# Performance work log

Measured on AMD Instinct MI355X. Metric: run time of the kernel, lower is better.

Reference implementation:

```python
import jax, jax.numpy as jnp
import numpy as np

SCALE = 2
STRIDE = 1


def setup_inputs() -> dict:
    key = jax.random.key(0)
    kx, kw, kb = jax.random.split(key, 3)
    B, Cin, H, W = 16, 128, 64, 64
    Cout, kh, kw_ = 128, 3, 3
    N = Cout * Cin * kh * kw_
    bound = 1.0 / np.sqrt(N)
    x = jax.random.normal(kx, (B, Cin, H, W), dtype=jnp.float32)
    weight = jax.random.uniform(kw, (Cout, Cin, kh, kw_), dtype=jnp.float32,
                                minval=-bound, maxval=bound)
    bias = jax.random.uniform(kb, (Cout,), dtype=jnp.float32,
                              minval=-bound, maxval=bound)
    return {"x": x, "weight": weight, "bias": bias}


def reference(x, weight, bias):
    # Nearest-neighbor upsample: each input pixel replicated SCALE x SCALE.
    up = jnp.repeat(jnp.repeat(x, SCALE, axis=2), SCALE, axis=3)  # [B,C,H*s,W*s]
    # Conv2d (cross-correlation, no padding), same math as unfold + matmul.
    out = jax.lax.conv_general_dilated(
        up, weight,
        window_strides=(STRIDE, STRIDE),
        padding="VALID",
        dimension_numbers=("NCHW", "OIHW", "NCHW"),
    )
    return out + bias[None, :, None, None]
```

## Files before the change

kernel.cpp:

```cpp
#include <hip/hip_runtime.h>
#include <hip/hip_bf16.h>
#include <stdint.h>


#define B_    16
#define CIN   128
#define HIN   64
#define WIN   64
#define COUT  128
#define HO    126
#define WO    126
#define M_TOT (B_ * 63 * 63)
#define BM    64
#define KTILES 16
#define AS_K  520

typedef __bf16 bf16;
typedef __bf16 bf16x8 __attribute__((ext_vector_type(8)));
typedef float  floatx4 __attribute__((ext_vector_type(4)));

__global__ void prep_weights(const float* __restrict__ w, bf16* __restrict__ wb) {
    int idx = blockIdx.x * 256 + threadIdx.x;
    if (idx >= 4 * KTILES * COUT * 32) return;
    int k32 = idx & 31;
    int o   = (idx >> 5) & 127;
    int par = (idx >> 12) & 3;
    int kt  = idx >> 14;
    int k = kt * 32 + k32;
    int c = k >> 2, u = (k >> 1) & 1, v = k & 1;
    int a = par >> 1, bp = par & 1;
    int dy0, dy1, ndy, dx0, dx1, ndx;
    if (u == 0) { if (a == 0) { dy0 = 0; dy1 = 1; ndy = 2; } else { dy0 = 0; dy1 = 0; ndy = 1; } }
    else        { if (a == 0) { dy0 = 2; dy1 = 2; ndy = 1; } else { dy0 = 1; dy1 = 2; ndy = 2; } }
    if (v == 0) { if (bp == 0) { dx0 = 0; dx1 = 1; ndx = 2; } else { dx0 = 0; dx1 = 0; ndx = 1; } }
    else        { if (bp == 0) { dx0 = 2; dx1 = 2; ndx = 1; } else { dx0 = 1; dx1 = 2; ndx = 2; } }
    const float* wp = w + (o * CIN + c) * 9;
    float s = wp[dy0 * 3 + dx0];
    if (ndx == 2) s += wp[dy0 * 3 + dx1];
    if (ndy == 2) { s += wp[dy1 * 3 + dx0]; if (ndx == 2) s += wp[dy1 * 3 + dx1]; }
    wb[idx] = (bf16)s;
}

__global__ __launch_bounds__(512, 4)
void upconv_gemm(const float* __restrict__ x, const bf16* __restrict__ wb,
                 const float* __restrict__ bias, float* __restrict__ out) {
    __shared__ bf16 As[BM * AS_K];
    float* Ld = reinterpret_cast<float*>(As);

    const int t    = threadIdx.x;
    const int lane = t & 63;
    const int wid  = t >> 6;
    const int a    = wid >> 2;
    const int oq   = wid & 3;
    const int quad = lane >> 4;
    const int l15  = lane & 15;
    const int kq   = quad * 8;

    const int m0 = blockIdx.x * BM;

    {
        const int ml = lane;
        const int m_mine = m0 + ml;
        const bool mvalid = (m_mine < M_TOT);
        int b_ = 0, p_ = 0, q_ = 0;
        if (mvalid) { b_ = m_mine / 3969; int rr = m_mine - b_ * 3969; p_ = rr / 63; q_ = rr - p_ * 63; }
        const float* xbase = x + ((b_ * CIN) * HIN + p_) * WIN + q_;

        #pragma unroll
        for (int j = 0; j < 8; ++j) {
            const int c0 = wid * 16 + 2 * j;
            float f0[4] = {0.f, 0.f, 0.f, 0.f}, f1[4] = {0.f, 0.f, 0.f, 0.f};
            if (mvalid) {
                const float* pa = xbase + c0 * (HIN * WIN);
                f0[0] = pa[0]; f0[1] = pa[1]; f0[2] = pa[WIN]; f0[3] = pa[WIN + 1];
                const float* pb = pa + (HIN * WIN);
                f1[0] = pb[0]; f1[1] = pb[1]; f1[2] = pb[WIN]; f1[3] = pb[WIN + 1];
            }
            bf16x8 v;
            v[0] = (bf16)f0[0]; v[1] = (bf16)f0[1]; v[2] = (bf16)f0[2]; v[3] = (bf16)f0[3];
            v[4] = (bf16)f1[0]; v[5] = (bf16)f1[1]; v[6] = (bf16)f1[2]; v[7] = (bf16)f1[3];
            const int g = wid * 8 + j;
            *(bf16x8*)&As[ml * AS_K + g * 8] = v;
        }
    }
    __syncthreads();

    const bf16* wwave = wb + ((a * 2) * COUT + oq * 32 + l15) * 32 + kq;

    floatx4 acc[2][4][2] = {};

    #pragma unroll
    for (int kt = 0; kt < KTILES; ++kt) {
        bf16x8 af[4], wf[2][2];
        #pragma unroll
        for (int i = 0; i < 4; ++i)
            af[i] = *(const bf16x8*)&As[(i * 16 + l15) * AS_K + kt * 32 + kq];
        #pragma unroll
        for (int bp = 0; bp < 2; ++bp)
            #pragma unroll
            for (int nt = 0; nt < 2; ++nt)
                wf[bp][nt] = *(const bf16x8*)(wwave
                    + (kt * 4 * COUT + bp * COUT + nt * 16) * 32);
        #pragma unroll
        for (int bp = 0; bp < 2; ++bp)
            #pragma unroll
            for (int mt = 0; mt < 4; ++mt)
                #pragma unroll
                for (int nt = 0; nt < 2; ++nt)
                    acc[bp][mt][nt] = __builtin_amdgcn_mfma_f32_16x16x32_bf16(
                        wf[bp][nt], af[mt], acc[bp][mt][nt], 0, 0, 0);
    }

    const int b_base = m0 / 3969;
    const int rr0 = m0 - b_base * 3969;
    const int p0  = rr0 / 63;
    const int q   = lane;

    #pragma unroll
    for (int ap = 0; ap < 2; ++ap) {
        __syncthreads();

        if (a == ap) {
            #pragma unroll
            for (int bp = 0; bp < 2; ++bp)
                #pragma unroll
                for (int mt = 0; mt < 4; ++mt)
                    #pragma unroll
                    for (int nt = 0; nt < 2; ++nt)
                        #pragma unroll
                        for (int ri = 0; ri < 4; ++ri) {
                            const int o   = oq * 32 + nt * 16 + quad * 4 + ri;
                            const int mlx = (mt * 16 + l15) ^ (quad << 4);
                            Ld[(o * 2 + bp) * 64 + mlx] = acc[bp][mt][nt][ri];
                        }
        }
        __syncthreads();

        for (int i = 0; i < 32; ++i) {
            const int rid = wid * 32 + i;
            const int o   = rid >> 1;
            const int pi  = rid & 1;
            int b = b_base, p = p0 + pi;
            if (p > 62) { b += 1; p = 0; }
            if (b >= B_) continue;
            const int base_m = b * 3969 + p * 63;
            const float bo = bias[o];
            const int m_lane = base_m + q;
            const bool val = (q < 63) && (m_lane >= m0) && (m_lane < m0 + BM) && (m_lane < M_TOT);
            if (val) {
                const int mloc = m_lane - m0;
                const int xsw  = ((o >> 2) & 3) << 4;
                const float v0 = Ld[(o * 2 + 0) * 64 + (mloc ^ xsw)];
                const float v1 = Ld[(o * 2 + 1) * 64 + (mloc ^ xsw)];
                const int y = 2 * p + ap;
                float* dst = out + b * (COUT * HO * WO) + o * (HO * WO) + y * WO + 2 * q;
                *(float2*)dst = make_float2(v0 + bo, v1 + bo);
            }
        }
    }
}

extern "C" void kernel_launch(void* const* d_in, const int* in_sizes, int n_in,
                              void* d_out, int out_size, void* d_ws, size_t ws_size,
                              hipStream_t stream) {
    const float* x    = (const float*)d_in[0];
    const float* w    = (const float*)d_in[1];
    const float* bias = (const float*)d_in[2];
    float* out = (float*)d_out;
    bf16* wb = (bf16*)d_ws;

    prep_weights<<<(4 * KTILES * COUT * 32 + 255) / 256, 256, 0, stream>>>(w, wb);

    dim3 grid((M_TOT + BM - 1) / BM);
    upconv_gemm<<<grid, 512, 0, stream>>>(x, wb, bias, out);
}
```

Baseline: 214.3 us.

## Double-buffer weights and activations in LDS with async global-to-LDS loads

Replaces the up-front full-K activation staging and the direct global weight loads with a double-buffered K loop. Each iteration streams the next weight tile into LDS with global_load_lds, using an XOR swizzle, and prefetches the next 8 input channels into registers, writing them into the alternate LDS buffer after the MFMAs. The aim is to overlap global memory latency with the matrix math and to cut per-wave redundant global weight reads. In exchange it adds a __syncthreads per K tile, uses more LDS (about 74KB), which may lower occupancy, and relies on the swizzle matching between prep layout and reads.

Measured after the change: 213.6 us. Within noise of the previous version (-0.3%).

```diff
diff --git a/kernel.cpp b/kernel.cpp
--- a/kernel.cpp
+++ b/kernel.cpp
@@ -13,9 +13,12 @@
 #define M_TOT (B_ * 63 * 63)
 #define BM    64
 #define KTILES 16
-#define AS_K  520
+#define WS_ELEMS 16384
+#define AS_STRIDE 40
+#define AS_ELEMS (64 * AS_STRIDE)
 
 typedef __bf16 bf16;
+typedef __bf16 bf16x4 __attribute__((ext_vector_type(4)));
 typedef __bf16 bf16x8 __attribute__((ext_vector_type(8)));
 typedef float  floatx4 __attribute__((ext_vector_type(4)));
 
@@ -44,8 +47,10 @@
 __global__ __launch_bounds__(512, 4)
 void upconv_gemm(const float* __restrict__ x, const bf16* __restrict__ wb,
                  const float* __restrict__ bias, float* __restrict__ out) {
-    __shared__ bf16 As[BM * AS_K];
-    float* Ld = reinterpret_cast<float*>(As);
+    __shared__ __align__(16) char smem[2 * WS_ELEMS * 2 + 2 * AS_ELEMS * 2];
+    bf16*  Ws  = (bf16*)smem;
+    bf16*  Asl = (bf16*)(smem + 2 * WS_ELEMS * 2);
+    float* Ld  = (float*)smem;
 
     const int t    = threadIdx.x;
     const int lane = t & 63;
@@ -58,49 +63,65 @@
 
     const int m0 = blockIdx.x * BM;
 
+    const int m_mine = m0 + lane;
+    const bool mvalid = (m_mine < M_TOT);
+    int b_ = 0, p_ = 0, q_ = 0;
+    if (mvalid) { b_ = m_mine / 3969; int rr = m_mine - b_ * 3969; p_ = rr / 63; q_ = rr - p_ * 63; }
+    const float* xpl = x + ((b_ * CIN + wid) * HIN + p_) * WIN + q_;
+
+    const int go_base = a * 1024 + oq * 128 + l15 * 4 + quad;
+
     {
-        const int ml = lane;
-        const int m_mine = m0 + ml;
-        const bool mvalid = (m_mine < M_TOT);
-        int b_ = 0, p_ = 0, q_ = 0;
-        if (mvalid) { b_ = m_mine / 3969; int rr = m_mine - b_ * 3969; p_ = rr / 63; q_ = rr - p_ * 63; }
-        const float* xbase = x + ((b_ * CIN) * HIN + p_) * WIN + q_;
-
-        #pragma unroll
-        for (int j = 0; j < 8; ++j) {
-            const int c0 = wid * 16 + 2 * j;
-            float f0[4] = {0.f, 0.f, 0.f, 0.f}, f1[4] = {0.f, 0.f, 0.f, 0.f};
-            if (mvalid) {
-                const float* pa = xbase + c0 * (HIN * WIN);
-                f0[0] = pa[0]; f0[1] = pa[1]; f0[2] = pa[WIN]; f0[3] = pa[WIN + 1];
-                const float* pb = pa + (HIN * WIN);
-                f1[0] = pb[0]; f1[1] = pb[1]; f1[2] = pb[WIN]; f1[3] = pb[WIN + 1];
-            }
-            bf16x8 v;
-            v[0] = (bf16)f0[0]; v[1] = (bf16)f0[1]; v[2] = (bf16)f0[2]; v[3] = (bf16)f0[3];
-            v[4] = (bf16)f1[0]; v[5] = (bf16)f1[1]; v[6] = (bf16)f1[2]; v[7] = (bf16)f1[3];
-            const int g = wid * 8 + j;
-            *(bf16x8*)&As[ml * AS_K + g * 8] = v;
-        }
+        #pragma unroll
+        for (int i = 0; i < 4; ++i) {
+            const int j  = i * 512 + t;
+            const int js = j ^ ((j >> 3) & 7);
+            __builtin_amdgcn_global_load_lds(
+                (const __attribute__((address_space(1))) uint32_t*)(const void*)(wb + js * 8),
+                (__attribute__((address_space(3))) uint32_t*)(void*)(Ws + j * 8),
+                16, 0, 0);
+        }
+        float f0 = 0.f, f1 = 0.f, f2 = 0.f, f3 = 0.f;
+        if (mvalid) { f0 = xpl[0]; f1 = xpl[1]; f2 = xpl[WIN]; f3 = xpl[WIN + 1]; }
+        bf16x4 v; v[0] = (bf16)f0; v[1] = (bf16)f1; v[2] = (bf16)f2; v[3] = (bf16)f3;
+        *(bf16x4*)&Asl[lane * AS_STRIDE + wid * 4] = v;
     }
     __syncthreads();
 
-    const bf16* wwave = wb + ((a * 2) * COUT + oq * 32 + l15) * 32 + kq;
-
     floatx4 acc[2][4][2] = {};
 
-    #pragma unroll
+    #pragma unroll 2
     for (int kt = 0; kt < KTILES; ++kt) {
+        const int cur = kt & 1;
+        const int nxt = cur ^ 1;
+
+        float f0 = 0.f, f1 = 0.f, f2 = 0.f, f3 = 0.f;
+        if (kt < KTILES - 1) {
+            #pragma unroll
+            for (int i = 0; i < 4; ++i) {
+                const int j  = i * 512 + t;
+                const int js = j ^ ((j >> 3) & 7);
+                __builtin_amdgcn_global_load_lds(
+                    (const __attribute__((address_space(1))) uint32_t*)(const void*)(wb + (kt + 1) * WS_ELEMS + js * 8),
+                    (__attribute__((address_space(3))) uint32_t*)(void*)(Ws + nxt * WS_ELEMS + j * 8),
+                    16, 0, 0);
+            }
+            const float* pa = xpl + (kt + 1) * 8 * (HIN * WIN);
+            if (mvalid) { f0 = pa[0]; f1 = pa[1]; f2 = pa[WIN]; f3 = pa[WIN + 1]; }
+        }
+
         bf16x8 af[4], wf[2][2];
         #pragma unroll
         for (int i = 0; i < 4; ++i)
-            af[i] = *(const bf16x8*)&As[(i * 16 + l15) * AS_K + kt * 32 + kq];
+            af[i] = *(const bf16x8*)&Asl[cur * AS_ELEMS + (i * 16 + l15) * AS_STRIDE + kq];
         #pragma unroll
         for (int bp = 0; bp < 2; ++bp)
             #pragma unroll
-            for (int nt = 0; nt < 2; ++nt)
-                wf[bp][nt] = *(const bf16x8*)(wwave
-                    + (kt * 4 * COUT + bp * COUT + nt * 16) * 32);
+            for (int nt = 0; nt < 2; ++nt) {
+                const int go = go_base + bp * 512 + nt * 64;
+                const int s  = go ^ ((go >> 3) & 7);
+                wf[bp][nt] = *(const bf16x8*)&Ws[cur * WS_ELEMS + s * 8];
+            }
         #pragma unroll
         for (int bp = 0; bp < 2; ++bp)
             #pragma unroll
@@ -109,6 +130,12 @@
                 for (int nt = 0; nt < 2; ++nt)
                     acc[bp][mt][nt] = __builtin_amdgcn_mfma_f32_16x16x32_bf16(
                         wf[bp][nt], af[mt], acc[bp][mt][nt], 0, 0, 0);
+
+        if (kt < KTILES - 1) {
+            bf16x4 v; v[0] = (bf16)f0; v[1] = (bf16)f1; v[2] = (bf16)f2; v[3] = (bf16)f3;
+            *(bf16x4*)&Asl[nxt * AS_ELEMS + lane * AS_STRIDE + wid * 4] = v;
+        }
+        __syncthreads();
     }
 
     const int b_base = m0 / 3969;
```

## Align GEMM tiles to output rows and simplify epilogue stores

Applied to the files above, without the earlier changes.

Each block now handles exactly one input row (63 pixels) of one image instead of a flat 64-pixel M tile. This removes the per-lane div/mod index math and the tile-straddling validity checks. The epilogue adds bias in registers and writes float2 pairs to an LDS buffer padded to 65 entries per channel. The copy-out loop is unrolled over 16 channels per wave, with no row-boundary branching, and uses nontemporal stores. One of the 64 M lanes in each tile is wasted, and the block count rises slightly.

Result: no change. 212.4 us (-0.9%).

```diff
diff --git a/kernel.cpp b/kernel.cpp
--- a/kernel.cpp
+++ b/kernel.cpp
@@ -10,14 +10,14 @@
 #define COUT  128
 #define HO    126
 #define WO    126
-#define M_TOT (B_ * 63 * 63)
-#define BM    64
+#define BM    63
 #define KTILES 16
 #define AS_K  520
 
 typedef __bf16 bf16;
 typedef __bf16 bf16x8 __attribute__((ext_vector_type(8)));
 typedef float  floatx4 __attribute__((ext_vector_type(4)));
+typedef float  floatx2 __attribute__((ext_vector_type(2)));
 
 __global__ void prep_weights(const float* __restrict__ w, bf16* __restrict__ wb) {
     int idx = blockIdx.x * 256 + threadIdx.x;
@@ -44,8 +44,8 @@
 __global__ __launch_bounds__(512, 4)
 void upconv_gemm(const float* __restrict__ x, const bf16* __restrict__ wb,
                  const float* __restrict__ bias, float* __restrict__ out) {
-    __shared__ bf16 As[BM * AS_K];
-    float* Ld = reinterpret_cast<float*>(As);
+    __shared__ bf16 As[64 * AS_K];
+    floatx2* Ld2 = reinterpret_cast<floatx2*>(As);
 
     const int t    = threadIdx.x;
     const int lane = t & 63;
@@ -56,15 +56,13 @@
     const int l15  = lane & 15;
     const int kq   = quad * 8;
 
-    const int m0 = blockIdx.x * BM;
+    const int bid = blockIdx.x;
+    const int b   = bid / 63;
+    const int p   = bid - b * 63;
 
     {
-        const int ml = lane;
-        const int m_mine = m0 + ml;
-        const bool mvalid = (m_mine < M_TOT);
-        int b_ = 0, p_ = 0, q_ = 0;
-        if (mvalid) { b_ = m_mine / 3969; int rr = m_mine - b_ * 3969; p_ = rr / 63; q_ = rr - p_ * 63; }
-        const float* xbase = x + ((b_ * CIN) * HIN + p_) * WIN + q_;
+        const bool mvalid = (lane < 63);
+        const float* xbase = x + ((b * CIN) * HIN + p) * WIN + lane;
 
         #pragma unroll
         for (int j = 0; j < 8; ++j) {
@@ -80,7 +78,7 @@
             v[0] = (bf16)f0[0]; v[1] = (bf16)f0[1]; v[2] = (bf16)f0[2]; v[3] = (bf16)f0[3];
             v[4] = (bf16)f1[0]; v[5] = (bf16)f1[1]; v[6] = (bf16)f1[2]; v[7] = (bf16)f1[3];
             const int g = wid * 8 + j;
-            *(bf16x8*)&As[ml * AS_K + g * 8] = v;
+            *(bf16x8*)&As[lane * AS_K + g * 8] = v;
         }
     }
     __syncthreads();
@@ -111,10 +109,14 @@
                         wf[bp][nt], af[mt], acc[bp][mt][nt], 0, 0, 0);
     }
 
-    const int b_base = m0 / 3969;
-    const int rr0 = m0 - b_base * 3969;
-    const int p0  = rr0 / 63;
-    const int q   = lane;
+    float bv[2][4];
+    #pragma unroll
+    for (int nt = 0; nt < 2; ++nt)
+        #pragma unroll
+        for (int ri = 0; ri < 4; ++ri)
+            bv[nt][ri] = bias[oq * 32 + nt * 16 + quad * 4 + ri];
+
+    const int y0 = 2 * p;
 
     #pragma unroll
     for (int ap = 0; ap < 2; ++ap) {
@@ -122,39 +124,28 @@
 
         if (a == ap) {
             #pragma unroll
-            for (int bp = 0; bp < 2; ++bp)
+            for (int mt = 0; mt < 4; ++mt)
                 #pragma unroll
-                for (int mt = 0; mt < 4; ++mt)
+                for (int nt = 0; nt < 2; ++nt)
                     #pragma unroll
-                    for (int nt = 0; nt < 2; ++nt)
-                        #pragma unroll
-                        for (int ri = 0; ri < 4; ++ri) {
-                            const int o   = oq * 32 + nt * 16 + quad * 4 + ri;
-                            const int mlx = (mt * 16 + l15) ^ (quad << 4);
-                            Ld[(o * 2 + bp) * 64 + mlx] = acc[bp][mt][nt][ri];
-                        }
+                    for (int ri = 0; ri < 4; ++ri) {
+                        const int o = oq * 32 + nt * 16 + quad * 4 + ri;
+                        const int q = mt * 16 + l15;
+                        floatx2 r;
+                        r[0] = acc[0][mt][nt][ri] + bv[nt][ri];
+                        r[1] = acc[1][mt][nt][ri] + bv[nt][ri];
+                        Ld2[o * 65 + q] = r;
+                    }
         }
         __syncthreads();
 
-        for (int i = 0; i < 32; ++i) {
-            const int rid = wid * 32 + i;
-            const int o   = rid >> 1;
-            const int pi  = rid & 1;
-            int b = b_base, p = p0 + pi;
-            if (p > 62) { b += 1; p = 0; }
-            if (b >= B_) continue;
-            const int base_m = b * 3969 + p * 63;
-            const float bo = bias[o];
-            const int m_lane = base_m + q;
-            const bool val = (q < 63) && (m_lane >= m0) && (m_lane < m0 + BM) && (m_lane < M_TOT);
-            if (val) {
-                const int mloc = m_lane - m0;
-                const int xsw  = ((o >> 2) & 3) << 4;
-                const float v0 = Ld[(o * 2 + 0) * 64 + (mloc ^ xsw)];
-                const float v1 = Ld[(o * 2 + 1) * 64 + (mloc ^ xsw)];
-                const int y = 2 * p + ap;
-                float* dst = out + b * (COUT * HO * WO) + o * (HO * WO) + y * WO + 2 * q;
-                *(float2*)dst = make_float2(v0 + bo, v1 + bo);
+        #pragma unroll
+        for (int i = 0; i < 16; ++i) {
+            const int o = wid * 16 + i;
+            if (lane < 63) {
+                floatx2 v = Ld2[o * 65 + lane];
+                float* dst = out + ((b * COUT + o) * HO + (y0 + ap)) * WO + 2 * lane;
+                __builtin_nontemporal_store(v, (floatx2*)dst);
             }
         }
     }
@@ -171,6 +162,5 @@
 
     prep_weights<<<(4 * KTILES * COUT * 32 + 255) / 256, 256, 0, stream>>>(w, wb);
 
-    dim3 grid((M_TOT + BM - 1) / BM);
-    upconv_gemm<<<grid, 512, 0, stream>>>(x, wb, bias, out);
+    upconv_gemm<<<dim3(B_ * 63), 512, 0, stream>>>(x, wb, bias, out);
 }
```
